# Kernel optimization log

Hardware: AMD Instinct MI355X
Metric: run time of the kernel (lower is better)

## Reference

```python
import jax, jax.numpy as jnp
import numpy as np

B, D, S, FL, NH, FF = 8, 4096, 16, 3, 32, 16384
DPH = D // NH  # hidden_size_per_attention_head


def rmsnorm(x, w, eps=1e-6):
    return x * jax.lax.rsqrt(jnp.mean(x * x, axis=-1, keepdims=True) + eps) * w


def setup_inputs() -> dict:
    key = jax.random.key(0)
    ks = jax.random.split(key, 16)
    s = 0.02
    return {
        "x": jax.random.normal(ks[0], (B, 1, D), jnp.float32),
        "fir_state": jax.random.normal(ks[1], (B, 3 * D, FL - 1), jnp.float32),
        "iir_state": jax.random.normal(ks[2], (B, D, S), jnp.float32),
        "pre_norm_w": jnp.ones((D,), jnp.float32),
        "proj_w": jax.random.normal(ks[3], (D, 3 * D), jnp.float32) * s,
        "sf_weight": jax.random.normal(ks[4], (3 * D, FL), jnp.float32) * 0.3,  # short_filter_weight (squeezed)
        "sf_bias": jax.random.normal(ks[5], (3 * D,), jnp.float32) * s,
        "D_res": jax.random.normal(ks[6], (D,), jnp.float32) * 0.3,  # cascade.D residual term
        "residues": jax.random.normal(ks[7], (D, S), jnp.float32) * 0.3,
        "log_poles": -jax.random.uniform(ks[8], (D, S, 1), jnp.float32, 0.01, 2.0),  # stable poles in (0,1)
        "out_w": jax.random.normal(ks[9], (D, D), jnp.float32) * s,
        "out_b": jnp.zeros((D,), jnp.float32),
        "post_norm_w": jnp.ones((D,), jnp.float32),
        "mlp_w1": jax.random.normal(ks[10], (D, FF), jnp.float32) * s,
        "mlp_w3": jax.random.normal(ks[11], (D, FF), jnp.float32) * s,
        "mlp_w2": jax.random.normal(ks[12], (FF, D), jnp.float32) * s,
    }


def reference(x, fir_state, iir_state, pre_norm_w, proj_w, sf_weight, sf_bias,
              D_res, residues, log_poles, out_w, out_b, post_norm_w,
              mlp_w1, mlp_w3, mlp_w2):
    # ---- projections on pre-normed input, take last token ----
    z = rmsnorm(x, pre_norm_w) @ proj_w          # (B, 1, 3D)
    u = z[:, -1]                                  # (B, 3D)
    # ---- single-step FIR (shift register), flip_filter=False, gated_bias=False ----
    cache = fir_state.shape[-1]                   # FL-1 = 2
    w = sf_weight[:, :cache + 1]                  # (3D, FL)
    h0, h = w[:, -1], w[:, :-1]
    z_pre = h0 * u + jnp.sum(fir_state * h, axis=-1) + sf_bias   # (B, 3D)
    new_fir = jnp.concatenate([fir_state[..., 1:], u[..., None]], axis=-1)
    # ---- column_split_hyena interleave/split ----
    b = z_pre.shape[0]
    z_r = z_pre.reshape(b, NH, 3 * DPH)
    x2 = z_r[:, :, :DPH].reshape(b, -1)
    x1 = z_r[:, :, DPH:2 * DPH].reshape(b, -1)
    v = z_r[:, :, 2 * DPH:].reshape(b, -1)
    # ---- diagonal IIR pole/residue state update ----
    x1v = x1 * v                                  # (B, D)
    poles = jnp.exp(log_poles)[..., 0][None]      # (1, D, S)
    new_iir = poles * iir_state + x1v[..., None]  # (B, D, S)
    res_state = jnp.sum(residues[None] * new_iir, axis=-1)  # (B, D)
    y = x2 * (res_state + D_res * x1v)            # (B, D)
    y = y[:, None]                                # (B, 1, D)
    # ---- out projection + residual, then SwiGLU MLP + residual ----
    x = y @ out_w + out_b + x
    xn = rmsnorm(x, post_norm_w)
    x = x + (jax.nn.silu(xn @ mlp_w1) * (xn @ mlp_w3)) @ mlp_w2
    return x, new_fir, new_iir
```

## Files before the change

kernel.cpp:

```cpp
#include <hip/hip_runtime.h>
#include <hip/hip_bf16.h>
#include <math.h>

#define BB 8
#define DD 4096
#define SS 16
#define NHH 32
#define FFF 16384
#define DPH 128
#define D3 12288

#define WS_Z     0
#define WS_XW    98304
#define WS_A1    131072
#define WS_A3    262144
#define WS_XD    393216
#define WS_ZERO_COUNT 425984
#define WS_XN1   425984
#define WS_Y     458752
#define WS_XATTN 491520
#define WS_XN2   524288
#define WS_G     557056

__global__ __launch_bounds__(256) void rmsnorm1_k(const float* __restrict__ x,
                                                  const float* __restrict__ w,
                                                  float* __restrict__ xn) {
    const int b = blockIdx.x;
    const int tid = threadIdx.x;
    float ss = 0.f;
    for (int d = tid; d < DD; d += 256) { float v = x[b*DD + d]; ss += v*v; }
    __shared__ float red[4];
    #pragma unroll
    for (int o = 32; o > 0; o >>= 1) ss += __shfl_down(ss, o);
    if ((tid & 63) == 0) red[tid >> 6] = ss;
    __syncthreads();
    float total = red[0] + red[1] + red[2] + red[3];
    float scale = rsqrtf(total / (float)DD + 1e-6f);
    for (int d = tid; d < DD; d += 256) xn[b*DD + d] = x[b*DD + d] * scale * w[d];
}

template<int RPB, int M>
__global__ __launch_bounds__(256) void gemv8_k(const float* __restrict__ X,
                                               const float* __restrict__ W,
                                               float* __restrict__ out, int N) {
    __shared__ float xs[BB][RPB];
    const int tid  = threadIdx.x;
    const int col  = blockIdx.x * 512 + tid * 2;
    const int row0 = blockIdx.y * RPB;
    for (int idx = tid; idx < BB * RPB; idx += 256) {
        int b = idx / RPB, r = idx - b * RPB;
        xs[b][r] = X[b * N + row0 + r];
    }
    __syncthreads();
    float acc[BB][2] = {};
    const float* Wp = W + (size_t)row0 * M + col;
    for (int r = 0; r < RPB; r += 4) {
        float2 w0 = *(const float2*)(Wp);
        float2 w1 = *(const float2*)(Wp + M);
        float2 w2 = *(const float2*)(Wp + 2 * (size_t)M);
        float2 w3 = *(const float2*)(Wp + 3 * (size_t)M);
        Wp += 4 * (size_t)M;
        #pragma unroll
        for (int b = 0; b < BB; ++b) {
            float4 xv = *(const float4*)&xs[b][r];
            acc[b][0] += xv.x*w0.x + xv.y*w1.x + xv.z*w2.x + xv.w*w3.x;
            acc[b][1] += xv.x*w0.y + xv.y*w1.y + xv.z*w2.y + xv.w*w3.y;
        }
    }
    #pragma unroll
    for (int b = 0; b < BB; ++b) {
        atomicAdd(&out[b * M + col],     acc[b][0]);
        atomicAdd(&out[b * M + col + 1], acc[b][1]);
    }
}

template<int RPB, int M>
__global__ __launch_bounds__(256) void gemv8_dual_k(const float* __restrict__ X,
                                                    const float* __restrict__ W1,
                                                    const float* __restrict__ W3,
                                                    float* __restrict__ o1,
                                                    float* __restrict__ o3, int N) {
    __shared__ float xs[BB][RPB];
    const int tid  = threadIdx.x;
    const int col  = blockIdx.x * 512 + tid * 2;
    const int row0 = blockIdx.y * RPB;
    for (int idx = tid; idx < BB * RPB; idx += 256) {
        int b = idx / RPB, r = idx - b * RPB;
        xs[b][r] = X[b * N + row0 + r];
    }
    __syncthreads();
    float acc1[BB][2] = {};
    float acc3[BB][2] = {};
    const float* W1p = W1 + (size_t)row0 * M + col;
    const float* W3p = W3 + (size_t)row0 * M + col;
    for (int r = 0; r < RPB; r += 2) {
        float2 a0 = *(const float2*)(W1p);
        float2 a1 = *(const float2*)(W1p + M);
        float2 b0 = *(const float2*)(W3p);
        float2 b1 = *(const float2*)(W3p + M);
        W1p += 2 * (size_t)M;
        W3p += 2 * (size_t)M;
        #pragma unroll
        for (int b = 0; b < BB; ++b) {
            float2 xv = *(const float2*)&xs[b][r];
            acc1[b][0] += xv.x*a0.x + xv.y*a1.x;
            acc1[b][1] += xv.x*a0.y + xv.y*a1.y;
            acc3[b][0] += xv.x*b0.x + xv.y*b1.x;
            acc3[b][1] += xv.x*b0.y + xv.y*b1.y;
        }
    }
    #pragma unroll
    for (int b = 0; b < BB; ++b) {
        atomicAdd(&o1[b * M + col],     acc1[b][0]);
        atomicAdd(&o1[b * M + col + 1], acc1[b][1]);
        atomicAdd(&o3[b * M + col],     acc3[b][0]);
        atomicAdd(&o3[b * M + col + 1], acc3[b][1]);
    }
}

__global__ __launch_bounds__(256) void fir_iir_k(const float* __restrict__ z,
                                                 const float* __restrict__ fir_state,
                                                 const float* __restrict__ iir_state,
                                                 const float* __restrict__ sf_weight,
                                                 const float* __restrict__ sf_bias,
                                                 const float* __restrict__ D_res,
                                                 const float* __restrict__ residues,
                                                 const float* __restrict__ log_poles,
                                                 float* __restrict__ new_fir,
                                                 float* __restrict__ new_iir,
                                                 float* __restrict__ y) {
    const int i = blockIdx.x * 256 + threadIdx.x;
    const int b = i >> 12;
    const int d = i & (DD - 1);
    const int h = d >> 7;
    const int p = d & (DPH - 1);
    const int j0 = h * (3 * DPH) + p;
    float zp[3];
    #pragma unroll
    for (int k = 0; k < 3; ++k) {
        int j = j0 + k * DPH;
        float u  = z[b * D3 + j];
        float f0 = fir_state[(b * D3 + j) * 2 + 0];
        float f1 = fir_state[(b * D3 + j) * 2 + 1];
        zp[k] = sf_weight[j*3+2] * u + f0 * sf_weight[j*3+0] + f1 * sf_weight[j*3+1] + sf_bias[j];
        new_fir[(b * D3 + j) * 2 + 0] = f1;
        new_fir[(b * D3 + j) * 2 + 1] = u;
    }
    float x2 = zp[0], x1 = zp[1], v = zp[2];
    float x1v = x1 * v;
    float res = 0.f;
    #pragma unroll
    for (int s = 0; s < SS; ++s) {
        float pole = expf(log_poles[d * SS + s]);
        float ni = pole * iir_state[(b * DD + d) * SS + s] + x1v;
        new_iir[(b * DD + d) * SS + s] = ni;
        res += residues[d * SS + s] * ni;
    }
    y[b * DD + d] = x2 * (res + D_res[d] * x1v);
}

__global__ __launch_bounds__(256) void post_k(const float* __restrict__ xw,
                                              const float* __restrict__ out_b,
                                              const float* __restrict__ x,
                                              const float* __restrict__ w,
                                              float* __restrict__ xattn,
                                              float* __restrict__ xn2) {
    const int b = blockIdx.x;
    const int tid = threadIdx.x;
    float ss = 0.f;
    for (int d = tid; d < DD; d += 256) {
        float v = xw[b*DD + d] + out_b[d] + x[b*DD + d];
        xattn[b*DD + d] = v;
        ss += v*v;
    }
    __shared__ float red[4];
    #pragma unroll
    for (int o = 32; o > 0; o >>= 1) ss += __shfl_down(ss, o);
    if ((tid & 63) == 0) red[tid >> 6] = ss;
    __syncthreads();
    float total = red[0] + red[1] + red[2] + red[3];
    float scale = rsqrtf(total / (float)DD + 1e-6f);
    for (int d = tid; d < DD; d += 256) xn2[b*DD + d] = xattn[b*DD + d] * scale * w[d];
}

__global__ __launch_bounds__(256) void gate_k(const float* __restrict__ a1,
                                              const float* __restrict__ a3,
                                              float* __restrict__ g) {
    const int i = blockIdx.x * 256 + threadIdx.x;
    float v = a1[i];
    float s = v / (1.f + expf(-v));
    g[i] = s * a3[i];
}

__global__ __launch_bounds__(256) void final_k(const float* __restrict__ xd,
                                               const float* __restrict__ xattn,
                                               float* __restrict__ out) {
    const int i = blockIdx.x * 256 + threadIdx.x;
    out[i] = xd[i] + xattn[i];
}

extern "C" void kernel_launch(void* const* d_in, const int* in_sizes, int n_in,
                              void* d_out, int out_size, void* d_ws, size_t ws_size,
                              hipStream_t stream) {
    const float* x         = (const float*)d_in[0];
    const float* fir_state = (const float*)d_in[1];
    const float* iir_state = (const float*)d_in[2];
    const float* pre_w     = (const float*)d_in[3];
    const float* proj_w    = (const float*)d_in[4];
    const float* sf_weight = (const float*)d_in[5];
    const float* sf_bias   = (const float*)d_in[6];
    const float* D_res     = (const float*)d_in[7];
    const float* residues  = (const float*)d_in[8];
    const float* log_poles = (const float*)d_in[9];
    const float* out_w     = (const float*)d_in[10];
    const float* out_b     = (const float*)d_in[11];
    const float* post_w    = (const float*)d_in[12];
    const float* mlp_w1    = (const float*)d_in[13];
    const float* mlp_w3    = (const float*)d_in[14];
    const float* mlp_w2    = (const float*)d_in[15];

    float* ws = (float*)d_ws;
    float* z     = ws + WS_Z;
    float* xw    = ws + WS_XW;
    float* a1    = ws + WS_A1;
    float* a3    = ws + WS_A3;
    float* xd    = ws + WS_XD;
    float* xn1   = ws + WS_XN1;
    float* y     = ws + WS_Y;
    float* xattn = ws + WS_XATTN;
    float* xn2   = ws + WS_XN2;
    float* g     = ws + WS_G;

    float* out_x   = (float*)d_out;
    float* new_fir = out_x + BB * DD;
    float* new_iir = new_fir + BB * D3 * 2;

    hipMemsetAsync(ws, 0, (size_t)WS_ZERO_COUNT * sizeof(float), stream);

    rmsnorm1_k<<<BB, 256, 0, stream>>>(x, pre_w, xn1);

    gemv8_k<256, D3><<<dim3(D3/512, DD/256), 256, 0, stream>>>(xn1, proj_w, z, DD);

    fir_iir_k<<<(BB*DD)/256, 256, 0, stream>>>(z, fir_state, iir_state, sf_weight,
                                               sf_bias, D_res, residues, log_poles,
                                               new_fir, new_iir, y);

    gemv8_k<128, DD><<<dim3(DD/512, DD/128), 256, 0, stream>>>(y, out_w, xw, DD);

    post_k<<<BB, 256, 0, stream>>>(xw, out_b, x, post_w, xattn, xn2);

    gemv8_dual_k<256, FFF><<<dim3(FFF/512, DD/256), 256, 0, stream>>>(xn2, mlp_w1, mlp_w3,
                                                                      a1, a3, DD);

    gate_k<<<(BB*FFF)/256, 256, 0, stream>>>(a1, a3, g);

    gemv8_k<512, DD><<<dim3(DD/512, FFF/512), 256, 0, stream>>>(g, mlp_w2, xd, FFF);

    final_k<<<(BB*DD)/256, 256, 0, stream>>>(xd, xattn, out_x);
}
```

Before: 935.7 us.

## Fuse gate and residual epilogues into GEMVs and widen loads to float4

Widens each thread's GEMV tile from 2 to 4 columns, using float4 weight loads with matching grid and row-split changes. Folds the SiLU gate into the down-projection's shared-memory load and seeds the residual plus bias into atomic accumulation targets, which removes the gate_k and final_k launches and their intermediate buffers. The down-projection now accumulates atomically straight into the output buffer, which post_k pre-fills with the attention residual. The gate is recomputed redundantly by each column block, and larger per-thread tiles raise register pressure.

```diff
diff --git a/kernel.cpp b/kernel.cpp
--- a/kernel.cpp
+++ b/kernel.cpp
@@ -1,5 +1,4 @@
 #include <hip/hip_runtime.h>
-#include <hip/hip_bf16.h>
 #include <math.h>
 
 #define BB 8
@@ -11,20 +10,19 @@
 #define D3 12288
 
 #define WS_Z     0
-#define WS_XW    98304
-#define WS_A1    131072
-#define WS_A3    262144
-#define WS_XD    393216
-#define WS_ZERO_COUNT 425984
-#define WS_XN1   425984
-#define WS_Y     458752
-#define WS_XATTN 491520
-#define WS_XN2   524288
-#define WS_G     557056
+#define WS_A1    98304
+#define WS_A3    229376
+#define WS_ZERO_COUNT 360448
+#define WS_XN1   360448
+#define WS_Y     393216
+#define WS_XW    425984
+#define WS_XN2   458752
 
 __global__ __launch_bounds__(256) void rmsnorm1_k(const float* __restrict__ x,
                                                   const float* __restrict__ w,
-                                                  float* __restrict__ xn) {
+                                                  const float* __restrict__ out_b,
+                                                  float* __restrict__ xn,
+                                                  float* __restrict__ xw_seed) {
     const int b = blockIdx.x;
     const int tid = threadIdx.x;
     float ss = 0.f;
@@ -36,7 +34,11 @@
     __syncthreads();
     float total = red[0] + red[1] + red[2] + red[3];
     float scale = rsqrtf(total / (float)DD + 1e-6f);
-    for (int d = tid; d < DD; d += 256) xn[b*DD + d] = x[b*DD + d] * scale * w[d];
+    for (int d = tid; d < DD; d += 256) {
+        float v = x[b*DD + d];
+        xn[b*DD + d] = v * scale * w[d];
+        xw_seed[b*DD + d] = v + out_b[d];
+    }
 }
 
 template<int RPB, int M>
@@ -45,32 +47,38 @@
                                                float* __restrict__ out, int N) {
     __shared__ float xs[BB][RPB];
     const int tid  = threadIdx.x;
-    const int col  = blockIdx.x * 512 + tid * 2;
+    const int col  = blockIdx.x * 1024 + tid * 4;
     const int row0 = blockIdx.y * RPB;
     for (int idx = tid; idx < BB * RPB; idx += 256) {
         int b = idx / RPB, r = idx - b * RPB;
         xs[b][r] = X[b * N + row0 + r];
     }
     __syncthreads();
-    float acc[BB][2] = {};
+    float4 acc[BB];
+    #pragma unroll
+    for (int b = 0; b < BB; ++b) acc[b] = make_float4(0.f, 0.f, 0.f, 0.f);
     const float* Wp = W + (size_t)row0 * M + col;
     for (int r = 0; r < RPB; r += 4) {
-        float2 w0 = *(const float2*)(Wp);
-        float2 w1 = *(const float2*)(Wp + M);
-        float2 w2 = *(const float2*)(Wp + 2 * (size_t)M);
-        float2 w3 = *(const float2*)(Wp + 3 * (size_t)M);
+        float4 w0 = *(const float4*)(Wp);
+        float4 w1 = *(const float4*)(Wp + M);
+        float4 w2 = *(const float4*)(Wp + 2 * (size_t)M);
+        float4 w3 = *(const float4*)(Wp + 3 * (size_t)M);
         Wp += 4 * (size_t)M;
         #pragma unroll
         for (int b = 0; b < BB; ++b) {
             float4 xv = *(const float4*)&xs[b][r];
-            acc[b][0] += xv.x*w0.x + xv.y*w1.x + xv.z*w2.x + xv.w*w3.x;
-            acc[b][1] += xv.x*w0.y + xv.y*w1.y + xv.z*w2.y + xv.w*w3.y;
+            acc[b].x += xv.x*w0.x + xv.y*w1.x + xv.z*w2.x + xv.w*w3.x;
+            acc[b].y += xv.x*w0.y + xv.y*w1.y + xv.z*w2.y + xv.w*w3.y;
+            acc[b].z += xv.x*w0.z + xv.y*w1.z + xv.z*w2.z + xv.w*w3.z;
+            acc[b].w += xv.x*w0.w + xv.y*w1.w + xv.z*w2.w + xv.w*w3.w;
         }
     }
     #pragma unroll
     for (int b = 0; b < BB; ++b) {
-        atomicAdd(&out[b * M + col],     acc[b][0]);
-        atomicAdd(&out[b * M + col + 1], acc[b][1]);
+        atomicAdd(&out[b * M + col],     acc[b].x);
+        atomicAdd(&out[b * M + col + 1], acc[b].y);
+        atomicAdd(&out[b * M + col + 2], acc[b].z);
+        atomicAdd(&out[b * M + col + 3], acc[b].w);
     }
 }
 
@@ -82,39 +90,95 @@
                                                     float* __restrict__ o3, int N) {
     __shared__ float xs[BB][RPB];
     const int tid  = threadIdx.x;
-    const int col  = blockIdx.x * 512 + tid * 2;
+    const int col  = blockIdx.x * 1024 + tid * 4;
     const int row0 = blockIdx.y * RPB;
     for (int idx = tid; idx < BB * RPB; idx += 256) {
         int b = idx / RPB, r = idx - b * RPB;
         xs[b][r] = X[b * N + row0 + r];
     }
     __syncthreads();
-    float acc1[BB][2] = {};
-    float acc3[BB][2] = {};
+    float4 acc1[BB], acc3[BB];
+    #pragma unroll
+    for (int b = 0; b < BB; ++b) {
+        acc1[b] = make_float4(0.f, 0.f, 0.f, 0.f);
+        acc3[b] = make_float4(0.f, 0.f, 0.f, 0.f);
+    }
     const float* W1p = W1 + (size_t)row0 * M + col;
     const float* W3p = W3 + (size_t)row0 * M + col;
     for (int r = 0; r < RPB; r += 2) {
-        float2 a0 = *(const float2*)(W1p);
-        float2 a1 = *(const float2*)(W1p + M);
-        float2 b0 = *(const float2*)(W3p);
-        float2 b1 = *(const float2*)(W3p + M);
+        float4 u0 = *(const float4*)(W1p);
+        float4 u1 = *(const float4*)(W1p + M);
+        float4 v0 = *(const float4*)(W3p);
+        float4 v1 = *(const float4*)(W3p + M);
         W1p += 2 * (size_t)M;
         W3p += 2 * (size_t)M;
         #pragma unroll
         for (int b = 0; b < BB; ++b) {
             float2 xv = *(const float2*)&xs[b][r];
-            acc1[b][0] += xv.x*a0.x + xv.y*a1.x;
-            acc1[b][1] += xv.x*a0.y + xv.y*a1.y;
-            acc3[b][0] += xv.x*b0.x + xv.y*b1.x;
-            acc3[b][1] += xv.x*b0.y + xv.y*b1.y;
+            acc1[b].x += xv.x*u0.x + xv.y*u1.x;
+            acc1[b].y += xv.x*u0.y + xv.y*u1.y;
+            acc1[b].z += xv.x*u0.z + xv.y*u1.z;
+            acc1[b].w += xv.x*u0.w + xv.y*u1.w;
+            acc3[b].x += xv.x*v0.x + xv.y*v1.x;
+            acc3[b].y += xv.x*v0.y + xv.y*v1.y;
+            acc3[b].z += xv.x*v0.z + xv.y*v1.z;
+            acc3[b].w += xv.x*v0.w + xv.y*v1.w;
         }
     }
     #pragma unroll
     for (int b = 0; b < BB; ++b) {
-        atomicAdd(&o1[b * M + col],     acc1[b][0]);
-        atomicAdd(&o1[b * M + col + 1], acc1[b][1]);
-        atomicAdd(&o3[b * M + col],     acc3[b][0]);
-        atomicAdd(&o3[b * M + col + 1], acc3[b][1]);
+        atomicAdd(&o1[b * M + col],     acc1[b].x);
+        atomicAdd(&o1[b * M + col + 1], acc1[b].y);
+        atomicAdd(&o1[b * M + col + 2], acc1[b].z);
+        atomicAdd(&o1[b * M + col + 3], acc1[b].w);
+        atomicAdd(&o3[b * M + col],     acc3[b].x);
+        atomicAdd(&o3[b * M + col + 1], acc3[b].y);
+        atomicAdd(&o3[b * M + col + 2], acc3[b].z);
+        atomicAdd(&o3[b * M + col + 3], acc3[b].w);
+    }
+}
+
+template<int RPB, int M>
+__global__ __launch_bounds__(256) void gemv8_gate_k(const float* __restrict__ A1,
+                                                    const float* __restrict__ A3,
+                                                    const float* __restrict__ W,
+                                                    float* __restrict__ out, int N) {
+    __shared__ float xs[BB][RPB];
+    const int tid  = threadIdx.x;
+    const int col  = blockIdx.x * 1024 + tid * 4;
+    const int row0 = blockIdx.y * RPB;
+    for (int idx = tid; idx < BB * RPB; idx += 256) {
+        int b = idx / RPB, r = idx - b * RPB;
+        float v1 = A1[b * N + row0 + r];
+        float v3 = A3[b * N + row0 + r];
+        xs[b][r] = v3 * (v1 / (1.f + expf(-v1)));
+    }
+    __syncthreads();
+    float4 acc[BB];
+    #pragma unroll
+    for (int b = 0; b < BB; ++b) acc[b] = make_float4(0.f, 0.f, 0.f, 0.f);
+    const float* Wp = W + (size_t)row0 * M + col;
+    for (int r = 0; r < RPB; r += 4) {
+        float4 w0 = *(const float4*)(Wp);
+        float4 w1 = *(const float4*)(Wp + M);
+        float4 w2 = *(const float4*)(Wp + 2 * (size_t)M);
+        float4 w3 = *(const float4*)(Wp + 3 * (size_t)M);
+        Wp += 4 * (size_t)M;
+        #pragma unroll
+        for (int b = 0; b < BB; ++b) {
+            float4 xv = *(const float4*)&xs[b][r];
+            acc[b].x += xv.x*w0.x + xv.y*w1.x + xv.z*w2.x + xv.w*w3.x;
+            acc[b].y += xv.x*w0.y + xv.y*w1.y + xv.z*w2.y + xv.w*w3.y;
+            acc[b].z += xv.x*w0.z + xv.y*w1.z + xv.z*w2.z + xv.w*w3.z;
+            acc[b].w += xv.x*w0.w + xv.y*w1.w + xv.z*w2.w + xv.w*w3.w;
+        }
+    }
+    #pragma unroll
+    for (int b = 0; b < BB; ++b) {
+        atomicAdd(&out[b * M + col],     acc[b].x);
+        atomicAdd(&out[b * M + col + 1], acc[b].y);
+        atomicAdd(&out[b * M + col + 2], acc[b].z);
+        atomicAdd(&out[b * M + col + 3], acc[b].w);
     }
 }
 
@@ -160,19 +224,13 @@
 }
 
 __global__ __launch_bounds__(256) void post_k(const float* __restrict__ xw,
-                                              const float* __restrict__ out_b,
-                                              const float* __restrict__ x,
                                               const float* __restrict__ w,
-                                              float* __restrict__ xattn,
+                                              float* __restrict__ out_x,
                                               float* __restrict__ xn2) {
     const int b = blockIdx.x;
     const int tid = threadIdx.x;
     float ss = 0.f;
-    for (int d = tid; d < DD; d += 256) {
-        float v = xw[b*DD + d] + out_b[d] + x[b*DD + d];
-        xattn[b*DD + d] = v;
-        ss += v*v;
-    }
+    for (int d = tid; d < DD; d += 256) { float v = xw[b*DD + d]; ss += v*v; }
     __shared__ float red[4];
     #pragma unroll
     for (int o = 32; o > 0; o >>= 1) ss += __shfl_down(ss, o);
@@ -180,23 +238,11 @@
     __syncthreads();
     float total = red[0] + red[1] + red[2] + red[3];
     float scale = rsqrtf(total / (float)DD + 1e-6f);
-    for (int d = tid; d < DD; d += 256) xn2[b*DD + d] = xattn[b*DD + d] * scale * w[d];
-}
-
-__global__ __launch_bounds__(256) void gate_k(const float* __restrict__ a1,
-                                              const float* __restrict__ a3,
-                                              float* __restrict__ g) {
-    const int i = blockIdx.x * 256 + threadIdx.x;
-    float v = a1[i];
-    float s = v / (1.f + expf(-v));
-    g[i] = s * a3[i];
-}
-
-__global__ __launch_bounds__(256) void final_k(const float* __restrict__ xd,
-                                               const float* __restrict__ xattn,
-                                               float* __restrict__ out) {
-    const int i = blockIdx.x * 256 + threadIdx.x;
-    out[i] = xd[i] + xattn[i];
+    for (int d = tid; d < DD; d += 256) {
+        float v = xw[b*DD + d];
+        out_x[b*DD + d] = v;
+        xn2[b*DD + d] = v * scale * w[d];
+    }
 }
 
 extern "C" void kernel_launch(void* const* d_in, const int* in_sizes, int n_in,
@@ -221,15 +267,12 @@
 
     float* ws = (float*)d_ws;
     float* z     = ws + WS_Z;
-    float* xw    = ws + WS_XW;
     float* a1    = ws + WS_A1;
     float* a3    = ws + WS_A3;
-    float* xd    = ws + WS_XD;
     float* xn1   = ws + WS_XN1;
     float* y     = ws + WS_Y;
-    float* xattn = ws + WS_XATTN;
+    float* xw    = ws + WS_XW;
     float* xn2   = ws + WS_XN2;
-    float* g     = ws + WS_G;
 
     float* out_x   = (float*)d_out;
     float* new_fir = out_x + BB * DD;
@@ -237,24 +280,21 @@
 
     hipMemsetAsync(ws, 0, (size_t)WS_ZERO_COUNT * sizeof(float), stream);
 
-    rmsnorm1_k<<<BB, 256, 0, stream>>>(x, pre_w, xn1);
-
-    gemv8_k<256, D3><<<dim3(D3/512, DD/256), 256, 0, stream>>>(xn1, proj_w, z, DD);
+    rmsnorm1_k<<<BB, 256, 0, stream>>>(x, pre_w, out_b, xn1, xw);
+
+    gemv8_k<128, D3><<<dim3(D3/1024, DD/128), 256, 0, stream>>>(xn1, proj_w, z, DD);
 
     fir_iir_k<<<(BB*DD)/256, 256, 0, stream>>>(z, fir_state, iir_state, sf_weight,
                                                sf_bias, D_res, residues, log_poles,
                                                new_fir, new_iir, y);
 
-    gemv8_k<128, DD><<<dim3(DD/512, DD/128), 256, 0, stream>>>(y, out_w, xw, DD);
-
-    post_k<<<BB, 256, 0, stream>>>(xw, out_b, x, post_w, xattn, xn2);
-
-    gemv8_dual_k<256, FFF><<<dim3(FFF/512, DD/256), 256, 0, stream>>>(xn2, mlp_w1, mlp_w3,
-                                                                      a1, a3, DD);
-
-    gate_k<<<(BB*FFF)/256, 256, 0, stream>>>(a1, a3, g);
-
-    gemv8_k<512, DD><<<dim3(DD/512, FFF/512), 256, 0, stream>>>(g, mlp_w2, xd, FFF);
-
-    final_k<<<(BB*DD)/256, 256, 0, stream>>>(xd, xattn, out_x);
-}
+    gemv8_k<64, DD><<<dim3(DD/1024, DD/64), 256, 0, stream>>>(y, out_w, xw, DD);
+
+    post_k<<<BB, 256, 0, stream>>>(xw, post_w, out_x, xn2);
+
+    gemv8_dual_k<256, FFF><<<dim3(FFF/1024, DD/256), 256, 0, stream>>>(xn2, mlp_w1, mlp_w3,
+                                                                       a1, a3, DD);
+
+    gemv8_gate_k<256, DD><<<dim3(DD/1024, FFF/256), 256, 0, stream>>>(a1, a3, mlp_w2,
+                                                                      out_x, FFF);
+}
```

Measured after the change: 1.103 ms. 17.9% more time.
